# Optimization experiments

Measured on AMD Instinct MI355X. Metric: run time of the kernel, lower is better.

The kernel has to match this reference:

```python
import jax, jax.numpy as jnp
import numpy as np

B, N, FDIM = 8, 2048, 256
ASSIGN_RATIO = 0.1
K = int(N * ASSIGN_RATIO) + 1  # num coarse nodes per graph (205)
DENSITY = 0.01


def setup_inputs() -> dict:
    key = jax.random.key(0)
    k1, k2, k3 = jax.random.split(key, 3)
    x = jax.random.normal(k1, (B, N, FDIM), dtype=jnp.float32)
    u = jax.random.uniform(k2, (B, N, N), dtype=jnp.float32)
    adj = jnp.where(u < DENSITY, u, 0.0)
    adj = 0.5 * (adj + jnp.swapaxes(adj, 1, 2))  # symmetric weighted adjacency
    W = jax.random.normal(k3, (FDIM, 1), dtype=jnp.float32) * 0.05
    b = jnp.zeros((1,), dtype=jnp.float32)
    return {"x": x, "adj": adj, "W": W, "b": b}


def _coarsen(x, adj, W, b):
    I = jnp.eye(N, dtype=adj.dtype)
    # --- GCNConv attention score (self-loops + symmetric normalization) ---
    A_hat = adj + I                       # [B,N,N]
    dg = A_hat.sum(-1) ** -0.5            # deg >= 1 via self-loop
    gcn_norm = dg[:, :, None] * A_hat * dg[:, None, :]
    alpha = jnp.einsum('bnm,bmf,fo->bno', gcn_norm, x, W) + b
    alpha = jax.nn.sigmoid(alpha ** 2)[..., 0]   # [B,N], sigmoid(gcn^2)
    # --- normalize_batch_adj: D^{-1/2}(A+I)D^{-1/2}, zero isolated rows ---
    d = jnp.clip(A_hat.sum(-1), 1.0, None) ** -0.5
    norm_adj = d[:, :, None] * A_hat * d[:, None, :]
    norm_adj = norm_adj * (adj.sum(-1) > 0).astype(adj.dtype)[:, :, None]
    # --- top-k cut on attention ---
    topv, topi = jax.lax.top_k(alpha, K)  # [B,K]
    cut = topv[:, K - 1]                  # k-th largest value per graph
    cut_alpha = jax.nn.relu(alpha + 1e-7 - cut[:, None])   # [B,N]
    # --- assignment matrix S = L1-row-normalized(norm_adj * cut_alpha_cols) ---
    S = norm_adj * cut_alpha[:, None, :]
    S = S / jnp.clip(jnp.abs(S).sum(-1, keepdims=True), 1e-12, None)
    # --- coarsening matmuls ---
    x_c = jnp.einsum('bnm,bnf->bmf', S, x)                 # S^T x
    coarse = jnp.einsum('bnm,bnk,bkl->bml', S, adj, S)     # S^T A S
    coarse = jnp.floor(coarse * 1e4) / 1e4                 # 4-digit truncation
    return x_c, coarse, S, topi


def reference(x, adj, W, b):
    return _coarsen(x, adj, W, b)
```

## Files before the change

### kernel.cpp

```cpp
#include <hip/hip_runtime.h>
#include <cstdint>
#include <cstddef>

#define BB 8
#define NN 2048
#define FD 256
#define KK 205
#define CAP 96
#define SELCAP 256

__global__ __launch_bounds__(256) void k_spy(const float* __restrict__ adj, const float* __restrict__ x,
                                             const float* __restrict__ W, int* __restrict__ ell_idx,
                                             float* __restrict__ ell_val, int* __restrict__ ell_cnt,
                                             float* __restrict__ dg, float* __restrict__ rowsum,
                                             float* __restrict__ y) {
  int r = blockIdx.x;
  const float* arow = adj + (size_t)r * NN;
  int t = threadIdx.x;
  float lv[8]; int li[8]; int lc = 0; float ls = 0.f;
#pragma unroll
  for (int j = 0; j < 8; ++j) {
    int m = t + j * 256;
    float v = arow[m];
    if (v != 0.f) { lv[lc] = v; li[lc] = m; ++lc; ls += v; }
  }
  __shared__ int cnts[256];
  __shared__ float ssum[256];
  cnts[t] = lc; ssum[t] = ls;
  __syncthreads();
  for (int off = 1; off < 256; off <<= 1) {
    int add = (t >= off) ? cnts[t - off] : 0;
    __syncthreads();
    cnts[t] += add;
    __syncthreads();
  }
  int start = cnts[t] - lc;
  size_t base = (size_t)r * CAP;
  for (int e = 0; e < lc; ++e) {
    int p = start + e;
    if (p < CAP) { ell_idx[base + p] = li[e]; ell_val[base + p] = lv[e]; }
  }
  for (int off = 128; off > 0; off >>= 1) {
    if (t < off) ssum[t] += ssum[t + off];
    __syncthreads();
  }
  if (t == 0) {
    int tot = cnts[255]; if (tot > CAP) tot = CAP;
    ell_cnt[r] = tot;
    float rs = ssum[0];
    rowsum[r] = rs;
    dg[r] = 1.0f / sqrtf(1.0f + rs);
  }
  __syncthreads();
  ssum[t] = x[(size_t)r * FD + t] * W[t];
  __syncthreads();
  for (int off = 128; off > 0; off >>= 1) {
    if (t < off) ssum[t] += ssum[t + off];
    __syncthreads();
  }
  if (t == 0) y[r] = ssum[0];
}

__global__ __launch_bounds__(256) void k_alpha(const int* __restrict__ ell_idx, const float* __restrict__ ell_val,
                                               const int* __restrict__ ell_cnt, const float* __restrict__ dg,
                                               const float* __restrict__ y, const float* __restrict__ bptr,
                                               float* __restrict__ alpha) {
  int lane = threadIdx.x & 63, wv = threadIdx.x >> 6;
  int r = blockIdx.x * 4 + wv;
  int b = r / NN;
  int cnt = ell_cnt[r];
  size_t base = (size_t)r * CAP;
  const float* dgb = dg + (size_t)b * NN;
  const float* yb = y + (size_t)b * NN;
  float acc = 0.f;
  for (int j = lane; j < cnt; j += 64) {
    int m = ell_idx[base + j];
    acc += ell_val[base + j] * dgb[m] * yb[m];
  }
#pragma unroll
  for (int off = 32; off > 0; off >>= 1) acc += __shfl_down(acc, off);
  if (lane == 0) {
    float dgn = dg[r];
    float z = dgn * (acc + dgn * y[r]) + bptr[0];
    float t2 = z * z;
    alpha[r] = 1.0f / (1.0f + expf(-t2));
  }
}

__global__ __launch_bounds__(256) void k_rank(const float* __restrict__ alpha, float* __restrict__ cutv,
                                              float* __restrict__ out_topi, int* __restrict__ sel_cnt) {
  __shared__ unsigned int keys[NN];
  int b = blockIdx.x & 7;
  int chunk = blockIdx.x >> 3;
  int t = threadIdx.x;
  if (chunk == 0 && t == 0) sel_cnt[b] = 0;
  const float* ab = alpha + (size_t)b * NN;
  for (int i = t; i < NN; i += 256) keys[i] = __float_as_uint(ab[i]);
  __syncthreads();
  int i = chunk * 256 + t;
  unsigned int ai = keys[i];
  int rank = 0;
  const uint4* k4 = (const uint4*)keys;
#pragma unroll 4
  for (int j4 = 0; j4 < NN / 4; ++j4) {
    uint4 v = k4[j4];
    int j = j4 * 4;
    rank += (v.x > ai) || (v.x == ai && (j + 0) < i);
    rank += (v.y > ai) || (v.y == ai && (j + 1) < i);
    rank += (v.z > ai) || (v.z == ai && (j + 2) < i);
    rank += (v.w > ai) || (v.w == ai && (j + 3) < i);
  }
  if (rank < KK) out_topi[(size_t)b * KK + rank] = (float)i;
  if (rank == KK - 1) cutv[b] = __uint_as_float(ai);
}

__global__ __launch_bounds__(256) void k_selcut(const float* __restrict__ alpha, const float* __restrict__ cutv,
                                                float* __restrict__ cutA, int* __restrict__ selidx,
                                                int* __restrict__ sel_list, int* __restrict__ sel_cnt) {
  int r = blockIdx.x * 256 + threadIdx.x;
  int b = r / NN, n = r % NN;
  float ca = fmaxf(alpha[r] + 1e-7f - cutv[b], 0.0f);
  cutA[r] = ca;
  int s = -1;
  if (ca > 0.f) {
    s = atomicAdd(&sel_cnt[b], 1);
    if (s < SELCAP) sel_list[b * SELCAP + s] = n; else s = -1;
  }
  selidx[r] = s;
}

__global__ __launch_bounds__(256) void k_sbuild(const int* __restrict__ ell_idx, const float* __restrict__ ell_val,
                                                const int* __restrict__ ell_cnt, const float* __restrict__ dg,
                                                const float* __restrict__ rowsum, const float* __restrict__ cutA,
                                                const int* __restrict__ selidx, float* __restrict__ inv_eff,
                                                float* __restrict__ Sc, float* __restrict__ outS) {
  __shared__ float row[NN];
  __shared__ float scrow[SELCAP];
  __shared__ int   sidx[CAP];
  __shared__ float sterm[CAP];
  __shared__ float red[256];
  __shared__ float s_inv, s_dv;
  int r = blockIdx.x;
  int b = r >> 11;
  int t = threadIdx.x;
#pragma unroll
  for (int j = 0; j < NN / 256; ++j) row[t + j * 256] = 0.f;
  if (t < SELCAP) scrow[t] = 0.f;
  int cnt = ell_cnt[r];
  size_t base = (size_t)r * CAP;
  float dgn = dg[r];
  const float* dgb = dg + (size_t)b * NN;
  const float* cab = cutA + (size_t)b * NN;
  const int* sib = selidx + (size_t)b * NN;
  float part = 0.f;
  for (int j = t; j < cnt; j += 256) {
    int m = ell_idx[base + j];
    float term = dgn * ell_val[base + j] * dgb[m] * cab[m];
    sidx[j] = m; sterm[j] = term;
    part += term;
  }
  red[t] = part;
  __syncthreads();
  for (int off = 128; off > 0; off >>= 1) {
    if (t < off) red[t] += red[t + off];
    __syncthreads();
  }
  if (t == 0) {
    float diag = dgn * dgn * cutA[r];
    float rho = red[0] + diag;
    float inv = (rowsum[r] > 0.f) ? (1.0f / fmaxf(rho, 1e-12f)) : 0.f;
    s_inv = inv; s_dv = diag * inv;
    inv_eff[r] = inv;
  }
  __syncthreads();
  float inv = s_inv;
  for (int j = t; j < cnt; j += 256) {
    float v = sterm[j] * inv;
    row[sidx[j]] = v;
    int si = sib[sidx[j]];
    if (si >= 0) scrow[si] = v;
  }
  __syncthreads();
  if (t == 0) {
    int n = r & (NN - 1);
    row[n] += s_dv;
    int si = sib[n];
    if (si >= 0) scrow[si] += s_dv;
  }
  __syncthreads();
  float4* dst = (float4*)(outS + (size_t)r * NN);
  const float4* src = (const float4*)row;
#pragma unroll
  for (int j = 0; j < NN / 4 / 256; ++j) dst[t + j * 256] = src[t + j * 256];
  if (t < SELCAP) Sc[(size_t)r * SELCAP + t] = scrow[t];
}

__global__ __launch_bounds__(256) void k_M(const int* __restrict__ ell_idx, const float* __restrict__ ell_val,
                                           const int* __restrict__ ell_cnt, const float* __restrict__ Sc,
                                           float* __restrict__ Mmat) {
  int b = blockIdx.x & 7;
  int n = blockIdx.x >> 3;
  int r = b * NN + n;
  int t = threadIdx.x;
  __shared__ int srk[CAP];
  __shared__ float sav[CAP];
  int cnt = ell_cnt[r];
  size_t base = (size_t)r * CAP;
  for (int e = t; e < cnt; e += 256) {
    srk[e] = b * NN + ell_idx[base + e];
    sav[e] = ell_val[base + e];
  }
  __syncthreads();
  float a0 = 0.f;
  for (int e = 0; e < cnt; ++e) a0 += sav[e] * Sc[(size_t)srk[e] * SELCAP + t];
  Mmat[(size_t)r * SELCAP + t] = a0;
}

__global__ __launch_bounds__(256) void k_epi(const float* __restrict__ x, const int* __restrict__ ell_idx,
                                             const float* __restrict__ ell_val, const int* __restrict__ ell_cnt,
                                             const float* __restrict__ dg, const float* __restrict__ cutA,
                                             const float* __restrict__ inv_eff, const int* __restrict__ sel_list,
                                             const int* __restrict__ sel_cnt, const float* __restrict__ Mmat,
                                             float* __restrict__ xc, float* __restrict__ coarse) {
  int b = blockIdx.x & 7;
  int i = blockIdx.x >> 3;
  int nsel = sel_cnt[b]; if (nsel > SELCAP) nsel = SELCAP;
  if (i >= nsel) return;
  int m = sel_list[b * SELCAP + i];
  int rm = b * NN + m;
  int cnt = ell_cnt[rm];
  size_t base = (size_t)rm * CAP;
  __shared__ int cn[CAP + 1];
  __shared__ float cw[CAP + 1];
  float dgm = dg[rm], cam = cutA[rm];
  for (int j = threadIdx.x; j <= cnt; j += 256) {
    if (j < cnt) {
      int n = ell_idx[base + j];
      cn[j] = b * NN + n;
      cw[j] = ell_val[base + j] * dg[b * NN + n] * dgm * cam * inv_eff[b * NN + n];
    } else {
      cn[j] = rm;
      cw[j] = dgm * dgm * cam * inv_eff[rm];
    }
  }
  __syncthreads();
  int t = threadIdx.x;
  float axc = 0.f, aco = 0.f;
  for (int e = 0; e <= cnt; ++e) {
    float w = cw[e];
    if (w == 0.f) continue;
    size_t rn = (size_t)cn[e];
    axc += w * x[rn * FD + t];
    aco += w * Mmat[rn * SELCAP + t];
  }
  xc[(size_t)rm * FD + t] = axc;
  if (t < nsel) {
    float* crow = coarse + (size_t)rm * NN;
    crow[sel_list[b * SELCAP + t]] = floorf(aco * 10000.0f) / 10000.0f;
  }
}

extern "C" void kernel_launch(void* const* d_in, const int* in_sizes, int n_in,
                              void* d_out, int out_size, void* d_ws, size_t ws_size,
                              hipStream_t stream) {
  (void)in_sizes; (void)n_in; (void)ws_size; (void)out_size;
  const float* x = (const float*)d_in[0];
  const float* adj = (const float*)d_in[1];
  const float* W = (const float*)d_in[2];
  const float* bptr = (const float*)d_in[3];

  float* out = (float*)d_out;
  const size_t XC_SZ = (size_t)BB * NN * FD;
  const size_t CO_SZ = (size_t)BB * NN * NN;
  const size_t S_SZ  = (size_t)BB * NN * NN;
  float* out_xc = out;
  float* out_co = out + XC_SZ;
  float* out_S  = out + XC_SZ + CO_SZ;
  float* out_ti = out + XC_SZ + CO_SZ + S_SZ;

  char* w = (char*)d_ws;
  int*   ell_idx = (int*)w;   w += (size_t)BB * NN * CAP * 4;
  float* ell_val = (float*)w; w += (size_t)BB * NN * CAP * 4;
  float* Sc      = (float*)w; w += (size_t)BB * NN * SELCAP * 4;
  float* Mmat    = (float*)w; w += (size_t)BB * NN * SELCAP * 4;
  int*   ell_cnt = (int*)w;   w += (size_t)BB * NN * 4;
  float* dg      = (float*)w; w += (size_t)BB * NN * 4;
  float* rowsum  = (float*)w; w += (size_t)BB * NN * 4;
  float* yv      = (float*)w; w += (size_t)BB * NN * 4;
  float* alpha   = (float*)w; w += (size_t)BB * NN * 4;
  float* cutA    = (float*)w; w += (size_t)BB * NN * 4;
  float* inv_eff = (float*)w; w += (size_t)BB * NN * 4;
  int*   selidx  = (int*)w;   w += (size_t)BB * NN * 4;
  float* cutv    = (float*)w; w += (size_t)BB * 4;
  int*   sel_cnt = (int*)w;   w += (size_t)BB * 4;
  int*   sel_list= (int*)w;   w += (size_t)BB * SELCAP * 4;

  hipMemsetAsync(out, 0, (XC_SZ + CO_SZ) * sizeof(float), stream);

  k_spy<<<BB * NN, 256, 0, stream>>>(adj, x, W, ell_idx, ell_val, ell_cnt, dg, rowsum, yv);
  k_alpha<<<BB * NN / 4, 256, 0, stream>>>(ell_idx, ell_val, ell_cnt, dg, yv, bptr, alpha);
  k_rank<<<BB * 8, 256, 0, stream>>>(alpha, cutv, out_ti, sel_cnt);
  k_selcut<<<BB * NN / 256, 256, 0, stream>>>(alpha, cutv, cutA, selidx, sel_list, sel_cnt);
  k_sbuild<<<BB * NN, 256, 0, stream>>>(ell_idx, ell_val, ell_cnt, dg, rowsum, cutA, selidx,
                                        inv_eff, Sc, out_S);
  k_M<<<BB * NN, 256, 0, stream>>>(ell_idx, ell_val, ell_cnt, Sc, Mmat);
  k_epi<<<BB * SELCAP, 256, 0, stream>>>(x, ell_idx, ell_val, ell_cnt, dg, cutA, inv_eff,
                                         sel_list, sel_cnt, Mmat, out_xc, out_co);
}
```

Measured before the change: 573.4 us.

## Replace memset with full-row epilogue writes and use atomic compaction plus shuffle reductions

Drops the large memset of the xc and coarse outputs. The epilogue now runs one block per row, builds each coarse row in shared memory and writes it out in full, zeros included, with float4 stores. In k_spy, the block-wide prefix scan used for ELL compaction is replaced by a shared-memory atomic counter, and the tree reductions in k_spy and k_sbuild become wavefront shuffle reductions. This removes a full extra write pass and many barriers. In exchange, the ELL entry order becomes nondeterministic and the epilogue launches many more blocks.

```diff
diff --git a/kernel.cpp b/kernel.cpp
--- a/kernel.cpp
+++ b/kernel.cpp
@@ -17,6 +17,11 @@
   int r = blockIdx.x;
   const float* arow = adj + (size_t)r * NN;
   int t = threadIdx.x;
+  int lane = t & 63, wv = t >> 6;
+  __shared__ int counter;
+  __shared__ float wsum[4], wy[4];
+  if (t == 0) counter = 0;
+  __syncthreads();
   float lv[8]; int li[8]; int lc = 0; float ls = 0.f;
 #pragma unroll
   for (int j = 0; j < 8; ++j) {
@@ -24,41 +29,30 @@
     float v = arow[m];
     if (v != 0.f) { lv[lc] = v; li[lc] = m; ++lc; ls += v; }
   }
-  __shared__ int cnts[256];
-  __shared__ float ssum[256];
-  cnts[t] = lc; ssum[t] = ls;
-  __syncthreads();
-  for (int off = 1; off < 256; off <<= 1) {
-    int add = (t >= off) ? cnts[t - off] : 0;
-    __syncthreads();
-    cnts[t] += add;
-    __syncthreads();
-  }
-  int start = cnts[t] - lc;
   size_t base = (size_t)r * CAP;
-  for (int e = 0; e < lc; ++e) {
-    int p = start + e;
-    if (p < CAP) { ell_idx[base + p] = li[e]; ell_val[base + p] = lv[e]; }
-  }
-  for (int off = 128; off > 0; off >>= 1) {
-    if (t < off) ssum[t] += ssum[t + off];
-    __syncthreads();
-  }
+  if (lc > 0) {
+    int start = atomicAdd(&counter, lc);
+    for (int e = 0; e < lc; ++e) {
+      int p = start + e;
+      if (p < CAP) { ell_idx[base + p] = li[e]; ell_val[base + p] = lv[e]; }
+    }
+  }
+#pragma unroll
+  for (int off = 32; off > 0; off >>= 1) ls += __shfl_down(ls, off);
+  if (lane == 0) wsum[wv] = ls;
+  float xv = x[(size_t)r * FD + t] * W[t];
+#pragma unroll
+  for (int off = 32; off > 0; off >>= 1) xv += __shfl_down(xv, off);
+  if (lane == 0) wy[wv] = xv;
+  __syncthreads();
   if (t == 0) {
-    int tot = cnts[255]; if (tot > CAP) tot = CAP;
+    int tot = counter; if (tot > CAP) tot = CAP;
     ell_cnt[r] = tot;
-    float rs = ssum[0];
+    float rs = wsum[0] + wsum[1] + wsum[2] + wsum[3];
     rowsum[r] = rs;
     dg[r] = 1.0f / sqrtf(1.0f + rs);
-  }
-  __syncthreads();
-  ssum[t] = x[(size_t)r * FD + t] * W[t];
-  __syncthreads();
-  for (int off = 128; off > 0; off >>= 1) {
-    if (t < off) ssum[t] += ssum[t + off];
-    __syncthreads();
-  }
-  if (t == 0) y[r] = ssum[0];
+    y[r] = wy[0] + wy[1] + wy[2] + wy[3];
+  }
 }
 
 __global__ __launch_bounds__(256) void k_alpha(const int* __restrict__ ell_idx, const float* __restrict__ ell_val,
@@ -138,11 +132,12 @@
   __shared__ float scrow[SELCAP];
   __shared__ int   sidx[CAP];
   __shared__ float sterm[CAP];
-  __shared__ float red[256];
+  __shared__ float wred[4];
   __shared__ float s_inv, s_dv;
   int r = blockIdx.x;
   int b = r >> 11;
   int t = threadIdx.x;
+  int lane = t & 63, wv = t >> 6;
 #pragma unroll
   for (int j = 0; j < NN / 256; ++j) row[t + j * 256] = 0.f;
   if (t < SELCAP) scrow[t] = 0.f;
@@ -159,15 +154,13 @@
     sidx[j] = m; sterm[j] = term;
     part += term;
   }
-  red[t] = part;
-  __syncthreads();
-  for (int off = 128; off > 0; off >>= 1) {
-    if (t < off) red[t] += red[t + off];
-    __syncthreads();
-  }
+#pragma unroll
+  for (int off = 32; off > 0; off >>= 1) part += __shfl_down(part, off);
+  if (lane == 0) wred[wv] = part;
+  __syncthreads();
   if (t == 0) {
     float diag = dgn * dgn * cutA[r];
-    float rho = red[0] + diag;
+    float rho = wred[0] + wred[1] + wred[2] + wred[3] + diag;
     float inv = (rowsum[r] > 0.f) ? (1.0f / fmaxf(rho, 1e-12f)) : 0.f;
     s_inv = inv; s_dv = diag * inv;
     inv_eff[r] = inv;
@@ -216,48 +209,57 @@
   Mmat[(size_t)r * SELCAP + t] = a0;
 }
 
-__global__ __launch_bounds__(256) void k_epi(const float* __restrict__ x, const int* __restrict__ ell_idx,
-                                             const float* __restrict__ ell_val, const int* __restrict__ ell_cnt,
-                                             const float* __restrict__ dg, const float* __restrict__ cutA,
-                                             const float* __restrict__ inv_eff, const int* __restrict__ sel_list,
-                                             const int* __restrict__ sel_cnt, const float* __restrict__ Mmat,
-                                             float* __restrict__ xc, float* __restrict__ coarse) {
+__global__ __launch_bounds__(256) void k_epi2(const float* __restrict__ x, const int* __restrict__ ell_idx,
+                                              const float* __restrict__ ell_val, const int* __restrict__ ell_cnt,
+                                              const float* __restrict__ dg, const float* __restrict__ cutA,
+                                              const float* __restrict__ inv_eff, const int* __restrict__ selidx,
+                                              const int* __restrict__ sel_list, const int* __restrict__ sel_cnt,
+                                              const float* __restrict__ Mmat,
+                                              float* __restrict__ xc, float* __restrict__ coarse) {
   int b = blockIdx.x & 7;
-  int i = blockIdx.x >> 3;
-  int nsel = sel_cnt[b]; if (nsel > SELCAP) nsel = SELCAP;
-  if (i >= nsel) return;
-  int m = sel_list[b * SELCAP + i];
+  int m = blockIdx.x >> 3;
   int rm = b * NN + m;
-  int cnt = ell_cnt[rm];
-  size_t base = (size_t)rm * CAP;
+  int t = threadIdx.x;
+  __shared__ float row[NN];
   __shared__ int cn[CAP + 1];
   __shared__ float cw[CAP + 1];
-  float dgm = dg[rm], cam = cutA[rm];
-  for (int j = threadIdx.x; j <= cnt; j += 256) {
-    if (j < cnt) {
-      int n = ell_idx[base + j];
-      cn[j] = b * NN + n;
-      cw[j] = ell_val[base + j] * dg[b * NN + n] * dgm * cam * inv_eff[b * NN + n];
-    } else {
-      cn[j] = rm;
-      cw[j] = dgm * dgm * cam * inv_eff[rm];
+#pragma unroll
+  for (int j = 0; j < NN / 256; ++j) row[t + j * 256] = 0.f;
+  bool sel = selidx[rm] >= 0;
+  int nsel = sel_cnt[b]; if (nsel > SELCAP) nsel = SELCAP;
+  int cnt = ell_cnt[rm];
+  if (sel) {
+    float dgm = dg[rm], cam = cutA[rm];
+    for (int j = t; j <= cnt; j += 256) {
+      if (j < cnt) {
+        int n = ell_idx[(size_t)rm * CAP + j];
+        cn[j] = b * NN + n;
+        cw[j] = ell_val[(size_t)rm * CAP + j] * dg[b * NN + n] * dgm * cam * inv_eff[b * NN + n];
+      } else {
+        cn[j] = rm;
+        cw[j] = dgm * dgm * cam * inv_eff[rm];
+      }
     }
   }
   __syncthreads();
-  int t = threadIdx.x;
-  float axc = 0.f, aco = 0.f;
-  for (int e = 0; e <= cnt; ++e) {
-    float w = cw[e];
-    if (w == 0.f) continue;
-    size_t rn = (size_t)cn[e];
-    axc += w * x[rn * FD + t];
-    aco += w * Mmat[rn * SELCAP + t];
+  float axc = 0.f;
+  if (sel) {
+    float aco = 0.f;
+    for (int e = 0; e <= cnt; ++e) {
+      float w = cw[e];
+      if (w == 0.f) continue;
+      size_t rn = (size_t)cn[e];
+      axc += w * x[rn * FD + t];
+      aco += w * Mmat[rn * SELCAP + t];
+    }
+    if (t < nsel) row[sel_list[b * SELCAP + t]] = floorf(aco * 10000.0f) / 10000.0f;
   }
   xc[(size_t)rm * FD + t] = axc;
-  if (t < nsel) {
-    float* crow = coarse + (size_t)rm * NN;
-    crow[sel_list[b * SELCAP + t]] = floorf(aco * 10000.0f) / 10000.0f;
-  }
+  __syncthreads();
+  float4* dst = (float4*)(coarse + (size_t)rm * NN);
+  const float4* src = (const float4*)row;
+#pragma unroll
+  for (int j = 0; j < NN / 4 / 256; ++j) dst[t + j * 256] = src[t + j * 256];
 }
 
 extern "C" void kernel_launch(void* const* d_in, const int* in_sizes, int n_in,
@@ -295,8 +297,6 @@
   int*   sel_cnt = (int*)w;   w += (size_t)BB * 4;
   int*   sel_list= (int*)w;   w += (size_t)BB * SELCAP * 4;
 
-  hipMemsetAsync(out, 0, (XC_SZ + CO_SZ) * sizeof(float), stream);
-
   k_spy<<<BB * NN, 256, 0, stream>>>(adj, x, W, ell_idx, ell_val, ell_cnt, dg, rowsum, yv);
   k_alpha<<<BB * NN / 4, 256, 0, stream>>>(ell_idx, ell_val, ell_cnt, dg, yv, bptr, alpha);
   k_rank<<<BB * 8, 256, 0, stream>>>(alpha, cutv, out_ti, sel_cnt);
@@ -304,6 +304,6 @@
   k_sbuild<<<BB * NN, 256, 0, stream>>>(ell_idx, ell_val, ell_cnt, dg, rowsum, cutA, selidx,
                                         inv_eff, Sc, out_S);
   k_M<<<BB * NN, 256, 0, stream>>>(ell_idx, ell_val, ell_cnt, Sc, Mmat);
-  k_epi<<<BB * SELCAP, 256, 0, stream>>>(x, ell_idx, ell_val, ell_cnt, dg, cutA, inv_eff,
-                                         sel_list, sel_cnt, Mmat, out_xc, out_co);
-}
+  k_epi2<<<BB * NN, 256, 0, stream>>>(x, ell_idx, ell_val, ell_cnt, dg, cutA, inv_eff,
+                                      selidx, sel_list, sel_cnt, Mmat, out_xc, out_co);
+}
```

Measured after the change: 565.7 us. Within noise of the previous version (-1.3%).
